# Performance work log

Measured on AMD Instinct MI355X. Metric: run time of the kernel, lower is better.

## Reference

```python
import jax, jax.numpy as jnp
import numpy as np

N, E = 100000, 400000
IN, HID, H, D = 165, 128, 8, 16  # per-head dim D = HID // H
NUM_CLASSES = 2


def layer_norm(x, g, b, eps=1e-5):
    m = jnp.mean(x, axis=-1, keepdims=True)
    v = jnp.var(x, axis=-1, keepdims=True)
    return (x - m) / jnp.sqrt(v + eps) * g + b


def transformer_conv(x, src, dst, Wq, bq, Wk, bk, Wv, bv, Ws, bs):
    # x: [N, HID]; src/dst: [E]
    n = x.shape[0]
    q = (x @ Wq + bq).reshape(n, H, D)
    k = (x @ Wk + bk).reshape(n, H, D)
    v = (x @ Wv + bv).reshape(n, H, D)
    # per-edge attention logits: [E, H]
    alpha = jnp.sum(q[dst] * k[src], axis=-1) / jnp.sqrt(jnp.float32(D))
    # segment softmax over incoming edges of each destination node
    amax = jax.ops.segment_max(alpha, dst, num_segments=n)          # [N, H]
    amax = jnp.where(jnp.isfinite(amax), amax, 0.0)
    ex = jnp.exp(alpha - amax[dst])                                  # [E, H]
    denom = jax.ops.segment_sum(ex, dst, num_segments=n)            # [N, H]
    a = ex / (denom[dst] + 1e-16)
    msg = v[src] * a[..., None]                                      # [E, H, D]
    out = jax.ops.segment_sum(msg, dst, num_segments=n)             # [N, H, D]
    out = out.reshape(n, H * D)
    # root skip connection (root_weight=True, beta=False in PyG defaults)
    return out + x @ Ws + bs


def setup_inputs() -> dict:
    key = jax.random.key(0)
    ks = jax.random.split(key, 24)
    rn = lambda k, s: (jax.random.normal(k, s, jnp.float32) * 0.05)
    inp = {
        "x": jax.random.normal(ks[0], (N, IN), jnp.float32),
        "edge_index": jax.random.randint(ks[1], (2, E), 0, N, jnp.int32),
        "W_in": rn(ks[2], (IN, HID)), "b_in": jnp.zeros((HID,), jnp.float32),
        # layer 1 TransformerConv
        "Wq1": rn(ks[3], (HID, HID)), "bq1": jnp.zeros((HID,), jnp.float32),
        "Wk1": rn(ks[4], (HID, HID)), "bk1": jnp.zeros((HID,), jnp.float32),
        "Wv1": rn(ks[5], (HID, HID)), "bv1": jnp.zeros((HID,), jnp.float32),
        "Ws1": rn(ks[6], (HID, HID)), "bs1": jnp.zeros((HID,), jnp.float32),
        "g1": jnp.ones((HID,), jnp.float32), "be1": jnp.zeros((HID,), jnp.float32),
        # layer 2 TransformerConv
        "Wq2": rn(ks[7], (HID, HID)), "bq2": jnp.zeros((HID,), jnp.float32),
        "Wk2": rn(ks[8], (HID, HID)), "bk2": jnp.zeros((HID,), jnp.float32),
        "Wv2": rn(ks[9], (HID, HID)), "bv2": jnp.zeros((HID,), jnp.float32),
        "Ws2": rn(ks[10], (HID, HID)), "bs2": jnp.zeros((HID,), jnp.float32),
        "g2": jnp.ones((HID,), jnp.float32), "be2": jnp.zeros((HID,), jnp.float32),
        # classifier MLP
        "Wc1": rn(ks[11], (HID, HID // 2)), "bc1": jnp.zeros((HID // 2,), jnp.float32),
        "Wc2": rn(ks[12], (HID // 2, NUM_CLASSES)), "bc2": jnp.zeros((NUM_CLASSES,), jnp.float32),
    }
    return inp


def reference(x, edge_index, W_in, b_in,
              Wq1, bq1, Wk1, bk1, Wv1, bv1, Ws1, bs1, g1, be1,
              Wq2, bq2, Wk2, bk2, Wv2, bv2, Ws2, bs2, g2, be2,
              Wc1, bc1, Wc2, bc2):
    src, dst = edge_index[0], edge_index[1]
    h = x @ W_in + b_in                                   # input projection
    h_new = transformer_conv(h, src, dst, Wq1, bq1, Wk1, bk1, Wv1, bv1, Ws1, bs1)
    h = layer_norm(h + h_new, g1, be1)                    # dropout = identity (eval)
    h_new = transformer_conv(h, src, dst, Wq2, bq2, Wk2, bk2, Wv2, bv2, Ws2, bs2)
    h = layer_norm(h + h_new, g2, be2)
    return jax.nn.relu(h @ Wc1 + bc1) @ Wc2 + bc2         # [N, num_classes]
```

## Files before the change

kernel.cpp:

```cpp
#include <hip/hip_runtime.h>
#include <hip/hip_bf16.h>

#define NN 100000
#define EE 400000
#define IN_DIM 165
#define KPAD 192
#define HID 128
#define C1 64
#define NC 2
#define SCANB 256
#define NBLK 391
#define NBD2 782

typedef const float* fpp;
typedef __hip_bfloat16 bf16;
typedef __attribute__((ext_vector_type(8))) short s16x8;
typedef __attribute__((ext_vector_type(4))) float f32x4;

__device__ __forceinline__ float bflo(unsigned u) { return __uint_as_float(u << 16); }
__device__ __forceinline__ float bfhi(unsigned u) { return __uint_as_float(u & 0xFFFF0000u); }
__device__ __forceinline__ unsigned short bfbits(float f) {
    bf16 h = __float2bfloat16(f);
    return *reinterpret_cast<unsigned short*>(&h);
}

__global__ void k_cvt_weights(fpp W_in, fpp Wq1, fpp Wk1, fpp Wv1, fpp Ws1,
                              fpp Wq2, fpp Wk2, fpp Wv2, fpp Ws2, fpp Wc1,
                              fpp bq1, fpp bk1, fpp bv1, fpp bs1,
                              fpp bq2, fpp bk2, fpp bv2, fpp bs2,
                              unsigned short* __restrict__ winpack,
                              unsigned short* __restrict__ wpack,
                              unsigned short* __restrict__ wc1t,
                              float* __restrict__ bpack) {
    int idx = blockIdx.x * blockDim.x + threadIdx.x;
    if (idx < 24576) {
        int n = idx / KPAD, k = idx % KPAD;
        float v = (k < IN_DIM) ? W_in[k * HID + n] : 0.f;
        winpack[idx] = bfbits(v);
    } else if (idx < 155648) {
        int local = idx - 24576;
        int layer = local >> 16;
        int rest = local & 65535;
        int chunk = rest >> 14;
        int l14 = rest & 16383;
        int n = l14 >> 7, k = l14 & 127;
        const float* src;
        int col;
        if (chunk == 0) { src = layer ? Wq2 : Wq1; col = n; }
        else if (chunk == 3) { src = layer ? Ws2 : Ws1; col = n; }
        else {
            int a = ((chunk == 2) ? 16 : 0) + (n >> 3), e = n & 7;
            src = (e < 4) ? (layer ? Wk2 : Wk1) : (layer ? Wv2 : Wv1);
            col = 4 * a + (e & 3);
        }
        wpack[local] = bfbits(src[k * HID + col]);
    } else if (idx < 163840) {
        int local = idx - 155648;
        int n = local >> 7, k = local & 127;
        wc1t[local] = bfbits(Wc1[k * C1 + n]);
    } else if (idx < 164864) {
        int local = idx - 163840;
        int layer = local >> 9;
        int rest = local & 511;
        int chunk = rest >> 7, n = rest & 127;
        const float* src;
        int col;
        if (chunk == 0) { src = layer ? bq2 : bq1; col = n; }
        else if (chunk == 3) { src = layer ? bs2 : bs1; col = n; }
        else {
            int a = ((chunk == 2) ? 16 : 0) + (n >> 3), e = n & 7;
            src = (e < 4) ? (layer ? bk2 : bk1) : (layer ? bv2 : bv1);
            col = 4 * a + (e & 3);
        }
        bpack[local] = src[col];
    }
}

__global__ void k_cvt_x(fpp x, unsigned short* __restrict__ xb) {
    int i = blockIdx.x * blockDim.x + threadIdx.x;
    int row = i / 24, c = i % 24;
    s16x8 us;
#pragma unroll
    for (int j = 0; j < 8; j++) {
        int col = c * 8 + j;
        float v = (col < IN_DIM) ? x[(size_t)row * IN_DIM + col] : 0.f;
        us[j] = (short)bfbits(v);
    }
    *(s16x8*)(xb + (size_t)row * KPAD + c * 8) = us;
}

__global__ void k_hist(const int* __restrict__ dst, int* __restrict__ deg) {
    int e = blockIdx.x * blockDim.x + threadIdx.x;
    if (e < EE) atomicAdd(&deg[dst[e]], 1);
}
__global__ void k_scan1(const int* __restrict__ deg, int* __restrict__ pos,
                        int* __restrict__ bsum, int n) {
    __shared__ int tmp[SCANB];
    int t = threadIdx.x, i = blockIdx.x * SCANB + t;
    int v = (i < n) ? deg[i] : 0;
    tmp[t] = v; __syncthreads();
    for (int off = 1; off < SCANB; off <<= 1) {
        int x = (t >= off) ? tmp[t - off] : 0;
        __syncthreads();
        tmp[t] += x;
        __syncthreads();
    }
    if (i < n) pos[i] = tmp[t] - v;
    if (t == SCANB - 1) bsum[blockIdx.x] = tmp[t];
}
__global__ void k_scan2(int* __restrict__ bsum, int nb) {
    __shared__ int tmp[512];
    int t = threadIdx.x;
    int v = (t < nb) ? bsum[t] : 0;
    tmp[t] = v; __syncthreads();
    for (int off = 1; off < 512; off <<= 1) {
        int x = (t >= off) ? tmp[t - off] : 0;
        __syncthreads();
        tmp[t] += x;
        __syncthreads();
    }
    if (t < nb) bsum[t] = tmp[t] - v;
}
__global__ void k_scan3(int* __restrict__ pos, const int* __restrict__ bsum,
                        const int* __restrict__ deg, int2* __restrict__ csr2, int n) {
    int i = blockIdx.x * blockDim.x + threadIdx.x;
    if (i < n) {
        int s = pos[i] + bsum[blockIdx.x];
        pos[i] = s;
        csr2[i] = make_int2(s, deg[i]);
    }
}
__global__ void k_fill(const int* __restrict__ src, const int* __restrict__ dst,
                       int* __restrict__ pos, int* __restrict__ esrc) {
    int e = blockIdx.x * blockDim.x + threadIdx.x;
    if (e < EE) {
        int p = atomicAdd(&pos[dst[e]], 1);
        esrc[p] = src[e];
    }
}

__global__ __launch_bounds__(256) void k_dense_in(const unsigned short* __restrict__ xb,
                                                  const unsigned short* __restrict__ winpack,
                                                  fpp b_in, unsigned short* __restrict__ hb) {
    __shared__ unsigned short smem[18432];
    unsigned short* As = smem;
    unsigned short* Ws = smem + 9216;
    int row0 = blockIdx.x * 128;
    int t = threadIdx.x, lane = t & 63, w = t >> 6;
    int quad = lane >> 4, l16 = lane & 15;
    int m_off = (w >> 1) * 64, n_off = (w & 1) * 64;

    f32x4 acc[4][4];
    float bias_v[4];
#pragma unroll
    for (int ni = 0; ni < 4; ni++) bias_v[ni] = b_in[n_off + ni * 16 + l16];
#pragma unroll
    for (int mi = 0; mi < 4; mi++)
#pragma unroll
        for (int ni = 0; ni < 4; ni++)
            acc[mi][ni] = (f32x4){bias_v[ni], bias_v[ni], bias_v[ni], bias_v[ni]};

    for (int kc = 0; kc < 3; kc++) {
        __syncthreads();
        for (int i = 0; i < 4; i++) {
            int g = t + i * 256;
            int r = g >> 3, c = g & 7;
            int rg = min(row0 + r, NN - 1);
            *(s16x8*)(As + r * 72 + c * 8) =
                *(const s16x8*)(xb + (size_t)rg * KPAD + kc * 64 + c * 8);
            *(s16x8*)(Ws + r * 72 + c * 8) =
                *(const s16x8*)(winpack + r * KPAD + kc * 64 + c * 8);
        }
        __syncthreads();
#pragma unroll
        for (int ks = 0; ks < 2; ks++) {
            int k0 = ks * 32;
            s16x8 a[4], b[4];
#pragma unroll
            for (int mi = 0; mi < 4; mi++)
                a[mi] = *(const s16x8*)(As + (m_off + mi * 16 + l16) * 72 + k0 + quad * 8);
#pragma unroll
            for (int ni = 0; ni < 4; ni++)
                b[ni] = *(const s16x8*)(Ws + (n_off + ni * 16 + l16) * 72 + k0 + quad * 8);
#pragma unroll
            for (int mi = 0; mi < 4; mi++)
#pragma unroll
                for (int ni = 0; ni < 4; ni++)
                    acc[mi][ni] = __builtin_amdgcn_mfma_f32_16x16x32_bf16(
                        a[mi], b[ni], acc[mi][ni], 0, 0, 0);
        }
    }
    __syncthreads();
    unsigned short* Cs = smem;
#pragma unroll
    for (int mi = 0; mi < 4; mi++)
#pragma unroll
        for (int ni = 0; ni < 4; ni++)
#pragma unroll
            for (int r = 0; r < 4; r++)
                Cs[(m_off + mi * 16 + quad * 4 + r) * 136 + n_off + ni * 16 + l16] =
                    bfbits(acc[mi][ni][r]);
    __syncthreads();
    for (int i = 0; i < 8; i++) {
        int g = t + i * 256;
        int r = g >> 4, c = g & 15;
        if (row0 + r < NN)
            *(s16x8*)(hb + (size_t)(row0 + r) * HID + c * 8) =
                *(const s16x8*)(Cs + r * 136 + c * 8);
    }
}

__global__ __launch_bounds__(256) void k_dense4(const unsigned short* __restrict__ hb,
                                                const unsigned short* __restrict__ wpackL,
                                                const float* __restrict__ bpackL,
                                                bf16* __restrict__ qb, bf16* __restrict__ kvb,
                                                bf16* __restrict__ agg) {
    __shared__ unsigned short As[128 * 136];
    __shared__ unsigned short Ws[128 * 136];
    int row0 = blockIdx.x * 128;
    int t = threadIdx.x, lane = t & 63, w = t >> 6;
    int quad = lane >> 4, l16 = lane & 15;
    int m_off = (w >> 1) * 64, n_off = (w & 1) * 64;

    for (int i = 0; i < 8; i++) {
        int g = t + i * 256;
        int r = g >> 4, c = g & 15;
        int rg = min(row0 + r, NN - 1);
        *(s16x8*)(As + r * 136 + c * 8) = *(const s16x8*)(hb + (size_t)rg * HID + c * 8);
    }
    __syncthreads();

    s16x8 afr[4][4];
#pragma unroll
    for (int ks = 0; ks < 4; ks++)
#pragma unroll
        for (int mi = 0; mi < 4; mi++)
            afr[ks][mi] = *(const s16x8*)(As + (m_off + mi * 16 + l16) * 136 + ks * 32 + quad * 8);

    for (int nc = 0; nc < 4; nc++) {
        unsigned short* tp; int stride;
        if (nc == 0)      { tp = (unsigned short*)qb;        stride = 128; }
        else if (nc == 1) { tp = (unsigned short*)kvb;       stride = 256; }
        else if (nc == 2) { tp = (unsigned short*)kvb + 128; stride = 256; }
        else              { tp = (unsigned short*)agg;       stride = 128; }
        const float* bp = bpackL + nc * 128;

        __syncthreads();
        for (int i = 0; i < 8; i++) {
            int g = t + i * 256;
            int r = g >> 4, c = g & 15;
            *(s16x8*)(Ws + r * 136 + c * 8) =
                *(const s16x8*)(wpackL + nc * 16384 + r * HID + c * 8);
        }
        __syncthreads();

        f32x4 acc[4][4];
        float bias_v[4];
#pragma unroll
        for (int ni = 0; ni < 4; ni++) bias_v[ni] = bp[n_off + ni * 16 + l16];
#pragma unroll
        for (int mi = 0; mi < 4; mi++)
#pragma unroll
            for (int ni = 0; ni < 4; ni++)
                acc[mi][ni] = (f32x4){bias_v[ni], bias_v[ni], bias_v[ni], bias_v[ni]};

#pragma unroll
        for (int ks = 0; ks < 4; ks++) {
            s16x8 b[4];
#pragma unroll
            for (int ni = 0; ni < 4; ni++)
                b[ni] = *(const s16x8*)(Ws + (n_off + ni * 16 + l16) * 136 + ks * 32 + quad * 8);
#pragma unroll
            for (int mi = 0; mi < 4; mi++)
#pragma unroll
                for (int ni = 0; ni < 4; ni++)
                    acc[mi][ni] = __builtin_amdgcn_mfma_f32_16x16x32_bf16(
                        afr[ks][mi], b[ni], acc[mi][ni], 0, 0, 0);
        }
        __syncthreads();

        unsigned short* Cs = Ws;
#pragma unroll
        for (int mi = 0; mi < 4; mi++)
#pragma unroll
            for (int ni = 0; ni < 4; ni++)
#pragma unroll
                for (int r = 0; r < 4; r++)
                    Cs[(m_off + mi * 16 + quad * 4 + r) * 136 + n_off + ni * 16 + l16] =
                        bfbits(acc[mi][ni][r]);
        __syncthreads();
        for (int i = 0; i < 8; i++) {
            int g = t + i * 256;
            int r = g >> 4, c = g & 15;
            if (row0 + r < NN)
                *(s16x8*)(tp + (size_t)(row0 + r) * stride + c * 8) =
                    *(const s16x8*)(Cs + r * 136 + c * 8);
        }
    }
}

__global__ void k_agg_ln(const bf16* __restrict__ qb, const bf16* __restrict__ kvb,
                         const int2* __restrict__ csr2, const int* __restrict__ esrc,
                         const bf16* __restrict__ agg, unsigned short* __restrict__ hb,
                         fpp g, fpp b) {
    int wv = (blockIdx.x * blockDim.x + threadIdx.x) >> 6;
    int lane = threadIdx.x & 63;
    int l32 = lane & 31;
    int d = wv * 2 + (lane >> 5);
    if (d >= NN) return;
    uint2 qu = ((const uint2*)(qb + (size_t)d * HID))[l32];
    float q0 = bflo(qu.x) * 0.25f, q1 = bfhi(qu.x) * 0.25f;
    float q2 = bflo(qu.y) * 0.25f, q3 = bfhi(qu.y) * 0.25f;
    int2 se = csr2[d];
    uint2 au = ((const uint2*)(agg + (size_t)d * HID))[l32];
    uint2 hu = ((const uint2*)(hb + (size_t)d * HID))[l32];
    float4 gv = ((const float4*)g)[l32];
    float4 bv = ((const float4*)b)[l32];
    int start = se.x, cnt = se.y;
    float m = -INFINITY, L = 0.f, o0 = 0.f, o1 = 0.f, o2 = 0.f, o3 = 0.f;
    for (int base = 0; base < cnt; base += 32) {
        int nc = min(32, cnt - base);
        int sj = (l32 < nc) ? esrc[start + base + l32] : 0;
        int j = 0;
        for (; j + 1 < nc; j += 2) {
            int s0 = __shfl(sj, j, 32);
            int s1 = __shfl(sj, j + 1, 32);
            uint4 kv0 = ((const uint4*)(kvb + (size_t)s0 * 256))[l32];
            uint4 kv1 = ((const uint4*)(kvb + (size_t)s1 * 256))[l32];
            float t0 = q0 * bflo(kv0.x) + q1 * bfhi(kv0.x) + q2 * bflo(kv0.y) + q3 * bfhi(kv0.y);
            float t1 = q0 * bflo(kv1.x) + q1 * bfhi(kv1.x) + q2 * bflo(kv1.y) + q3 * bfhi(kv1.y);
            t0 += __shfl_xor(t0, 1); t1 += __shfl_xor(t1, 1);
            t0 += __shfl_xor(t0, 2); t1 += __shfl_xor(t1, 2);
            float nm = fmaxf(m, fmaxf(t0, t1));
            float corr = __expf(m - nm);
            float p0 = __expf(t0 - nm), p1 = __expf(t1 - nm);
            L = L * corr + p0 + p1;
            o0 = o0 * corr + p0 * bflo(kv0.z) + p1 * bflo(kv1.z);
            o1 = o1 * corr + p0 * bfhi(kv0.z) + p1 * bfhi(kv1.z);
            o2 = o2 * corr + p0 * bflo(kv0.w) + p1 * bflo(kv1.w);
            o3 = o3 * corr + p0 * bfhi(kv0.w) + p1 * bfhi(kv1.w);
            m = nm;
        }
        if (j < nc) {
            int s0 = __shfl(sj, j, 32);
            uint4 kv0 = ((const uint4*)(kvb + (size_t)s0 * 256))[l32];
            float t0 = q0 * bflo(kv0.x) + q1 * bfhi(kv0.x) + q2 * bflo(kv0.y) + q3 * bfhi(kv0.y);
            t0 += __shfl_xor(t0, 1);
            t0 += __shfl_xor(t0, 2);
            float nm = fmaxf(m, t0);
            float corr = __expf(m - nm);
            float p0 = __expf(t0 - nm);
            L = L * corr + p0;
            o0 = o0 * corr + p0 * bflo(kv0.z);
            o1 = o1 * corr + p0 * bfhi(kv0.z);
            o2 = o2 * corr + p0 * bflo(kv0.w);
            o3 = o3 * corr + p0 * bfhi(kv0.w);
            m = nm;
        }
    }
    float inv = 1.f / (L + 1e-16f);
    float v0 = bflo(hu.x) + bflo(au.x) + o0 * inv;
    float v1 = bfhi(hu.x) + bfhi(au.x) + o1 * inv;
    float v2 = bflo(hu.y) + bflo(au.y) + o2 * inv;
    float v3 = bfhi(hu.y) + bfhi(au.y) + o3 * inv;
    float s = v0 + v1 + v2 + v3;
    float s2 = v0 * v0 + v1 * v1 + v2 * v2 + v3 * v3;
    for (int off = 16; off; off >>= 1) {
        s += __shfl_xor(s, off);
        s2 += __shfl_xor(s2, off);
    }
    float mn = s * (1.f / HID);
    float var = s2 * (1.f / HID) - mn * mn;
    float invs = rsqrtf(var + 1e-5f);
    float ox = (v0 - mn) * invs * gv.x + bv.x;
    float oy = (v1 - mn) * invs * gv.y + bv.y;
    float oz = (v2 - mn) * invs * gv.z + bv.z;
    float ow = (v3 - mn) * invs * gv.w + bv.w;
    uint2 outw;
    outw.x = ((unsigned)bfbits(oy) << 16) | bfbits(ox);
    outw.y = ((unsigned)bfbits(ow) << 16) | bfbits(oz);
    ((uint2*)(hb + (size_t)d * HID))[l32] = outw;
}

__global__ __launch_bounds__(256) void k_classifier(const unsigned short* __restrict__ hb,
                                                    const unsigned short* __restrict__ wc1t,
                                                    fpp bc1, fpp Wc2, fpp bc2,
                                                    float* __restrict__ out) {
    __shared__ unsigned short As[128 * 136];
    __shared__ unsigned short Ws[64 * 136];
    int row0 = blockIdx.x * 128;
    int t = threadIdx.x, lane = t & 63, w = t >> 6;
    int quad = lane >> 4, l16 = lane & 15;
    int m_off = w * 32;

    for (int i = 0; i < 8; i++) {
        int g = t + i * 256;
        int r = g >> 4, c = g & 15;
        int rg = min(row0 + r, NN - 1);
        *(s16x8*)(As + r * 136 + c * 8) = *(const s16x8*)(hb + (size_t)rg * HID + c * 8);
    }
    for (int i = 0; i < 4; i++) {
        int g = t + i * 256;
        int r = g >> 4, c = g & 15;
        *(s16x8*)(Ws + r * 136 + c * 8) = *(const s16x8*)(wc1t + r * HID + c * 8);
    }
    __syncthreads();

    f32x4 acc[2][4];
    float bias_v[4];
#pragma unroll
    for (int ni = 0; ni < 4; ni++) bias_v[ni] = bc1[ni * 16 + l16];
#pragma unroll
    for (int mi = 0; mi < 2; mi++)
#pragma unroll
        for (int ni = 0; ni < 4; ni++)
            acc[mi][ni] = (f32x4){bias_v[ni], bias_v[ni], bias_v[ni], bias_v[ni]};

#pragma unroll
    for (int ks = 0; ks < 4; ks++) {
        s16x8 a[2], b[4];
#pragma unroll
        for (int mi = 0; mi < 2; mi++)
            a[mi] = *(const s16x8*)(As + (m_off + mi * 16 + l16) * 136 + ks * 32 + quad * 8);
#pragma unroll
        for (int ni = 0; ni < 4; ni++)
            b[ni] = *(const s16x8*)(Ws + (ni * 16 + l16) * 136 + ks * 32 + quad * 8);
#pragma unroll
        for (int mi = 0; mi < 2; mi++)
#pragma unroll
            for (int ni = 0; ni < 4; ni++)
                acc[mi][ni] = __builtin_amdgcn_mfma_f32_16x16x32_bf16(
                    a[mi], b[ni], acc[mi][ni], 0, 0, 0);
    }
    __syncthreads();
    float* Cs = (float*)As;
#pragma unroll
    for (int mi = 0; mi < 2; mi++)
#pragma unroll
        for (int ni = 0; ni < 4; ni++)
#pragma unroll
            for (int r = 0; r < 4; r++)
                Cs[(m_off + mi * 16 + quad * 4 + r) * 68 + ni * 16 + l16] =
                    fmaxf(acc[mi][ni][r], 0.f);
    __syncthreads();

    int row = t >> 1, half = t & 1;
    float p0 = 0.f, p1 = 0.f;
    for (int c = half * 32; c < half * 32 + 32; c++) {
        float v = Cs[row * 68 + c];
        p0 += v * Wc2[c * NC + 0];
        p1 += v * Wc2[c * NC + 1];
    }
    p0 += __shfl_xor(p0, 1, 64);
    p1 += __shfl_xor(p1, 1, 64);
    if (half == 0 && row0 + row < NN) {
        out[(size_t)(row0 + row) * NC + 0] = p0 + bc2[0];
        out[(size_t)(row0 + row) * NC + 1] = p1 + bc2[1];
    }
}

extern "C" void kernel_launch(void* const* d_in, const int* in_sizes, int n_in,
                              void* d_out, int out_size, void* d_ws, size_t ws_size,
                              hipStream_t stream) {
    fpp x = (fpp)d_in[0];
    const int* ei = (const int*)d_in[1];
    const int* src = ei;
    const int* dst = ei + EE;
    fpp W_in = (fpp)d_in[2];  fpp b_in = (fpp)d_in[3];
    fpp Wq1 = (fpp)d_in[4];   fpp bq1 = (fpp)d_in[5];
    fpp Wk1 = (fpp)d_in[6];   fpp bk1 = (fpp)d_in[7];
    fpp Wv1 = (fpp)d_in[8];   fpp bv1 = (fpp)d_in[9];
    fpp Ws1 = (fpp)d_in[10];  fpp bs1 = (fpp)d_in[11];
    fpp g1 = (fpp)d_in[12];   fpp be1 = (fpp)d_in[13];
    fpp Wq2 = (fpp)d_in[14];  fpp bq2 = (fpp)d_in[15];
    fpp Wk2 = (fpp)d_in[16];  fpp bk2 = (fpp)d_in[17];
    fpp Wv2 = (fpp)d_in[18];  fpp bv2 = (fpp)d_in[19];
    fpp Ws2 = (fpp)d_in[20];  fpp bs2 = (fpp)d_in[21];
    fpp g2 = (fpp)d_in[22];   fpp be2 = (fpp)d_in[23];
    fpp Wc1 = (fpp)d_in[24];  fpp bc1 = (fpp)d_in[25];
    fpp Wc2 = (fpp)d_in[26];  fpp bc2 = (fpp)d_in[27];
    float* out = (float*)d_out;

    char* p = (char*)d_ws;
    unsigned short* hb = (unsigned short*)p;  p += (size_t)NN * HID * 2;
    bf16* agg = (bf16*)p;            p += (size_t)NN * HID * 2;
    bf16* qb = (bf16*)p;             p += (size_t)NN * HID * 2;
    bf16* kvb = (bf16*)p;            p += (size_t)NN * 256 * 2;
    int* deg = (int*)p;              p += (size_t)NN * 4;
    int* pos = (int*)p;              p += (size_t)NN * 4;
    int2* csr2 = (int2*)p;           p += (size_t)NN * 8;
    int* esrc = (int*)p;             p += (size_t)EE * 4;
    int* bsum = (int*)p;             p += 512 * 4;
    unsigned short* winpack = (unsigned short*)p;  p += 24576 * 2;
    unsigned short* wpack = (unsigned short*)p;    p += 131072 * 2;
    unsigned short* wc1t = (unsigned short*)p;     p += 8192 * 2;
    float* bpack = (float*)p;                      p += 1024 * 4;
    unsigned short* xb = (unsigned short*)qb;

    const int nE = (EE + 255) / 256;
    const int nNn = (NN + 255) / 256;

    k_cvt_weights<<<644, 256, 0, stream>>>(W_in, Wq1, Wk1, Wv1, Ws1,
                                           Wq2, Wk2, Wv2, Ws2, Wc1,
                                           bq1, bk1, bv1, bs1, bq2, bk2, bv2, bs2,
                                           winpack, wpack, wc1t, bpack);
    k_cvt_x<<<9375, 256, 0, stream>>>(x, xb);

    hipMemsetAsync(deg, 0, (size_t)NN * 4, stream);
    k_hist<<<nE, 256, 0, stream>>>(dst, deg);
    k_scan1<<<NBLK, SCANB, 0, stream>>>(deg, pos, bsum, NN);
    k_scan2<<<1, 512, 0, stream>>>(bsum, NBLK);
    k_scan3<<<NBLK, SCANB, 0, stream>>>(pos, bsum, deg, csr2, NN);
    k_fill<<<nE, 256, 0, stream>>>(src, dst, pos, esrc);

    k_dense_in<<<NBD2, 256, 0, stream>>>(xb, winpack, b_in, hb);

    for (int layer = 0; layer < 2; layer++) {
        fpp g = layer ? g2 : g1, be = layer ? be2 : be1;
        const unsigned short* wpackL = wpack + (size_t)layer * 65536;
        const float* bpackL = bpack + (size_t)layer * 512;

        k_dense4<<<NBD2, 256, 0, stream>>>(hb, wpackL, bpackL, qb, kvb, agg);
        k_agg_ln<<<12500, 256, 0, stream>>>(qb, kvb, csr2, esrc, agg, hb, g, be);
    }

    k_classifier<<<NBD2, 256, 0, stream>>>(hb, wc1t, bc1, Wc2, bc2, out);
}
```

Before: 404.1 us.

## Batch first eight edge gathers in attention aggregation and fold residual into GEMM epilogue

The aggregation kernel now issues up to eight K/V row gathers at once into registers, computes a two-pass max-then-exp softmax over them, and only falls back to the online-softmax loop for higher-degree nodes. This raises memory-level parallelism for typical low in-degree nodes. The residual h is also added into the skip-projection output inside the dense kernel epilogue (nc==3 path), which removes a separate read of hb in the aggregation kernel. In exchange, register pressure rises from holding eight uint4 loads, and the residual is rounded to bf16 one extra time.

```diff
diff --git a/kernel.cpp b/kernel.cpp
--- a/kernel.cpp
+++ b/kernel.cpp
@@ -19,6 +19,7 @@
 
 __device__ __forceinline__ float bflo(unsigned u) { return __uint_as_float(u << 16); }
 __device__ __forceinline__ float bfhi(unsigned u) { return __uint_as_float(u & 0xFFFF0000u); }
+__device__ __forceinline__ float us2f(unsigned short u) { return __uint_as_float((unsigned)u << 16); }
 __device__ __forceinline__ unsigned short bfbits(float f) {
     bf16 h = __float2bfloat16(f);
     return *reinterpret_cast<unsigned short*>(&h);
@@ -289,12 +290,29 @@
                     Cs[(m_off + mi * 16 + quad * 4 + r) * 136 + n_off + ni * 16 + l16] =
                         bfbits(acc[mi][ni][r]);
         __syncthreads();
-        for (int i = 0; i < 8; i++) {
-            int g = t + i * 256;
-            int r = g >> 4, c = g & 15;
-            if (row0 + r < NN)
-                *(s16x8*)(tp + (size_t)(row0 + r) * stride + c * 8) =
-                    *(const s16x8*)(Cs + r * 136 + c * 8);
+        if (nc == 3) {
+            for (int i = 0; i < 8; i++) {
+                int g = t + i * 256;
+                int r = g >> 4, c = g & 15;
+                if (row0 + r < NN) {
+                    s16x8 cv = *(const s16x8*)(Cs + r * 136 + c * 8);
+                    s16x8 hv = *(const s16x8*)(As + r * 136 + c * 8);
+                    s16x8 ov;
+#pragma unroll
+                    for (int j = 0; j < 8; j++)
+                        ov[j] = (short)bfbits(us2f((unsigned short)cv[j]) +
+                                              us2f((unsigned short)hv[j]));
+                    *(s16x8*)(tp + (size_t)(row0 + r) * stride + c * 8) = ov;
+                }
+            }
+        } else {
+            for (int i = 0; i < 8; i++) {
+                int g = t + i * 256;
+                int r = g >> 4, c = g & 15;
+                if (row0 + r < NN)
+                    *(s16x8*)(tp + (size_t)(row0 + r) * stride + c * 8) =
+                        *(const s16x8*)(Cs + r * 136 + c * 8);
+            }
         }
     }
 }
@@ -313,56 +331,81 @@
     float q2 = bflo(qu.y) * 0.25f, q3 = bfhi(qu.y) * 0.25f;
     int2 se = csr2[d];
     uint2 au = ((const uint2*)(agg + (size_t)d * HID))[l32];
-    uint2 hu = ((const uint2*)(hb + (size_t)d * HID))[l32];
     float4 gv = ((const float4*)g)[l32];
     float4 bv = ((const float4*)b)[l32];
     int start = se.x, cnt = se.y;
-    float m = -INFINITY, L = 0.f, o0 = 0.f, o1 = 0.f, o2 = 0.f, o3 = 0.f;
-    for (int base = 0; base < cnt; base += 32) {
+
+    int sj = (l32 < cnt) ? esrc[start + l32] : 0;
+
+    uint4 kv[8];
+    float tt[8];
+    float m = -INFINITY;
+#pragma unroll
+    for (int j = 0; j < 8; j++) {
+        int s = __shfl(sj, j, 32);
+        if (j < cnt) kv[j] = ((const uint4*)(kvb + (size_t)s * 256))[l32];
+        else kv[j] = (uint4){0u, 0u, 0u, 0u};
+        float t = q0 * bflo(kv[j].x) + q1 * bfhi(kv[j].x) +
+                  q2 * bflo(kv[j].y) + q3 * bfhi(kv[j].y);
+        t += __shfl_xor(t, 1);
+        t += __shfl_xor(t, 2);
+        tt[j] = (j < cnt) ? t : -INFINITY;
+        m = fmaxf(m, tt[j]);
+    }
+    if (cnt == 0) m = 0.f;
+    float L = 0.f, o0 = 0.f, o1 = 0.f, o2 = 0.f, o3 = 0.f;
+#pragma unroll
+    for (int j = 0; j < 8; j++) {
+        float p = __expf(tt[j] - m);
+        L += p;
+        o0 += p * bflo(kv[j].z);
+        o1 += p * bfhi(kv[j].z);
+        o2 += p * bflo(kv[j].w);
+        o3 += p * bfhi(kv[j].w);
+    }
+
+    for (int j = 8; j < min(cnt, 32); j++) {
+        int s = __shfl(sj, j, 32);
+        uint4 kvt = ((const uint4*)(kvb + (size_t)s * 256))[l32];
+        float t = q0 * bflo(kvt.x) + q1 * bfhi(kvt.x) + q2 * bflo(kvt.y) + q3 * bfhi(kvt.y);
+        t += __shfl_xor(t, 1);
+        t += __shfl_xor(t, 2);
+        float nm = fmaxf(m, t);
+        float corr = __expf(m - nm);
+        float p = __expf(t - nm);
+        L = L * corr + p;
+        o0 = o0 * corr + p * bflo(kvt.z);
+        o1 = o1 * corr + p * bfhi(kvt.z);
+        o2 = o2 * corr + p * bflo(kvt.w);
+        o3 = o3 * corr + p * bfhi(kvt.w);
+        m = nm;
+    }
+    for (int base = 32; base < cnt; base += 32) {
         int nc = min(32, cnt - base);
-        int sj = (l32 < nc) ? esrc[start + base + l32] : 0;
-        int j = 0;
-        for (; j + 1 < nc; j += 2) {
-            int s0 = __shfl(sj, j, 32);
-            int s1 = __shfl(sj, j + 1, 32);
-            uint4 kv0 = ((const uint4*)(kvb + (size_t)s0 * 256))[l32];
-            uint4 kv1 = ((const uint4*)(kvb + (size_t)s1 * 256))[l32];
-            float t0 = q0 * bflo(kv0.x) + q1 * bfhi(kv0.x) + q2 * bflo(kv0.y) + q3 * bfhi(kv0.y);
-            float t1 = q0 * bflo(kv1.x) + q1 * bfhi(kv1.x) + q2 * bflo(kv1.y) + q3 * bfhi(kv1.y);
-            t0 += __shfl_xor(t0, 1); t1 += __shfl_xor(t1, 1);
-            t0 += __shfl_xor(t0, 2); t1 += __shfl_xor(t1, 2);
-            float nm = fmaxf(m, fmaxf(t0, t1));
+        int sj2 = (l32 < nc) ? esrc[start + base + l32] : 0;
+        for (int j = 0; j < nc; j++) {
+            int s = __shfl(sj2, j, 32);
+            uint4 kvt = ((const uint4*)(kvb + (size_t)s * 256))[l32];
+            float t = q0 * bflo(kvt.x) + q1 * bfhi(kvt.x) + q2 * bflo(kvt.y) + q3 * bfhi(kvt.y);
+            t += __shfl_xor(t, 1);
+            t += __shfl_xor(t, 2);
+            float nm = fmaxf(m, t);
             float corr = __expf(m - nm);
-            float p0 = __expf(t0 - nm), p1 = __expf(t1 - nm);
-            L = L * corr + p0 + p1;
-            o0 = o0 * corr + p0 * bflo(kv0.z) + p1 * bflo(kv1.z);
-            o1 = o1 * corr + p0 * bfhi(kv0.z) + p1 * bfhi(kv1.z);
-            o2 = o2 * corr + p0 * bflo(kv0.w) + p1 * bflo(kv1.w);
-            o3 = o3 * corr + p0 * bfhi(kv0.w) + p1 * bfhi(kv1.w);
+            float p = __expf(t - nm);
+            L = L * corr + p;
+            o0 = o0 * corr + p * bflo(kvt.z);
+            o1 = o1 * corr + p * bfhi(kvt.z);
+            o2 = o2 * corr + p * bflo(kvt.w);
+            o3 = o3 * corr + p * bfhi(kvt.w);
             m = nm;
         }
-        if (j < nc) {
-            int s0 = __shfl(sj, j, 32);
-            uint4 kv0 = ((const uint4*)(kvb + (size_t)s0 * 256))[l32];
-            float t0 = q0 * bflo(kv0.x) + q1 * bfhi(kv0.x) + q2 * bflo(kv0.y) + q3 * bfhi(kv0.y);
-            t0 += __shfl_xor(t0, 1);
-            t0 += __shfl_xor(t0, 2);
-            float nm = fmaxf(m, t0);
-            float corr = __expf(m - nm);
-            float p0 = __expf(t0 - nm);
-            L = L * corr + p0;
-            o0 = o0 * corr + p0 * bflo(kv0.z);
-            o1 = o1 * corr + p0 * bfhi(kv0.z);
-            o2 = o2 * corr + p0 * bflo(kv0.w);
-            o3 = o3 * corr + p0 * bfhi(kv0.w);
-            m = nm;
-        }
-    }
+    }
+
     float inv = 1.f / (L + 1e-16f);
-    float v0 = bflo(hu.x) + bflo(au.x) + o0 * inv;
-    float v1 = bfhi(hu.x) + bfhi(au.x) + o1 * inv;
-    float v2 = bflo(hu.y) + bflo(au.y) + o2 * inv;
-    float v3 = bfhi(hu.y) + bfhi(au.y) + o3 * inv;
+    float v0 = bflo(au.x) + o0 * inv;
+    float v1 = bfhi(au.x) + o1 * inv;
+    float v2 = bflo(au.y) + o2 * inv;
+    float v3 = bfhi(au.y) + o3 * inv;
     float s = v0 + v1 + v2 + v3;
     float s2 = v0 * v0 + v1 * v1 + v2 * v2 + v3 * v3;
     for (int off = 16; off; off >>= 1) {
@@ -498,7 +541,6 @@
     unsigned short* xb = (unsigned short*)qb;
 
     const int nE = (EE + 255) / 256;
-    const int nNn = (NN + 255) / 256;
 
     k_cvt_weights<<<644, 256, 0, stream>>>(W_in, Wq1, Wk1, Wv1, Ws1,
                                            Wq2, Wk2, Wv2, Ws2, Wc1,
```

Result: no change. 406.0 us (+0.5%).
